# Performance work log

Measured on AMD Instinct MI355X. Metric: run time of the kernel, lower is better.

## Reference

```python
import jax, jax.numpy as jnp
import numpy as np
import math

N_HEADS = 16


def setup_inputs() -> dict:
    key = jax.random.key(0)
    ks = jax.random.split(key, 5)
    B, S, E = 2, 2048, 1024
    scale = 1.0 / math.sqrt(E)
    return {
        "x": jax.random.normal(ks[0], (B, S, E), dtype=jnp.float32),
        "w_in": jax.random.normal(ks[1], (3 * E, E), dtype=jnp.float32) * scale,
        "b_in": jax.random.normal(ks[2], (3 * E,), dtype=jnp.float32) * 0.01,
        "w_out": jax.random.normal(ks[3], (E, E), dtype=jnp.float32) * scale,
        "b_out": jax.random.normal(ks[4], (E,), dtype=jnp.float32) * 0.01,
    }


def reference(x, w_in, b_in, w_out, b_out):
    B, S, E = x.shape
    H = N_HEADS
    d = E // H
    # fused QKV projection: [B,S,3E]
    qkv = x @ w_in.T + b_in
    q, k, v = jnp.split(qkv, 3, axis=-1)
    # [B,S,E] -> [B,H,S,d]
    q = q.reshape(B, S, H, d).transpose(0, 2, 1, 3)
    k = k.reshape(B, S, H, d).transpose(0, 2, 1, 3)
    v = v.reshape(B, S, H, d).transpose(0, 2, 1, 3)
    # scores [B,H,S,S], scaled by 1/sqrt(d_head) (no causal mask: casual_mask=False)
    scores = jnp.einsum("bhqd,bhkd->bhqk", q, k) / jnp.sqrt(jnp.float32(d)).astype(x.dtype)
    w = jax.nn.softmax(scores, axis=-1)
    # attention output [B,H,S,d] -> [B,S,E]
    out = jnp.einsum("bhqk,bhkd->bhqd", w, v)
    out = out.transpose(0, 2, 1, 3).reshape(B, S, E)
    return out @ w_out.T + b_out
```

## Files before the change

kernel.cpp:

```cpp
#include <hip/hip_runtime.h>
#include <cstdint>


typedef __bf16 bf16x8 __attribute__((ext_vector_type(8)));
typedef short s16x4 __attribute__((ext_vector_type(4)));
typedef float f32x4 __attribute__((ext_vector_type(4)));

__device__ __forceinline__ unsigned short f32_to_bf16_rne(float f) {
    unsigned int u = __builtin_bit_cast(unsigned int, f);
    u += 0x7FFF + ((u >> 16) & 1);
    return (unsigned short)(u >> 16);
}

__device__ __forceinline__ unsigned int pack_bf16_trunc(float a, float b) {
    unsigned int ua = __builtin_bit_cast(unsigned int, a);
    unsigned int ub = __builtin_bit_cast(unsigned int, b);
    return __builtin_amdgcn_perm(ub, ua, 0x07060302u);
}

__device__ __forceinline__ void gload16(const void* g, void* l) {
    __builtin_amdgcn_global_load_lds(
        (const __attribute__((address_space(1))) unsigned int*)g,
        (__attribute__((address_space(3))) unsigned int*)l, 16, 0, 0);
}

__global__ void cvt_all(const float* __restrict__ x, const float* __restrict__ wi,
                        const float* __restrict__ wo, unsigned short* __restrict__ xb,
                        unsigned short* __restrict__ wib, unsigned short* __restrict__ wob) {
    int i = blockIdx.x * blockDim.x + threadIdx.x;
    const float* src; unsigned short* dst; int off;
    if (i < 1048576)            { src = x;  dst = xb;  off = i; }
    else if (i < 1048576 + 786432) { src = wi; dst = wib; off = i - 1048576; }
    else                        { src = wo; dst = wob; off = i - (1048576 + 786432); }
    float4 v = ((const float4*)src)[off];
    ushort4 o;
    o.x = f32_to_bf16_rne(v.x); o.y = f32_to_bf16_rne(v.y);
    o.z = f32_to_bf16_rne(v.z); o.w = f32_to_bf16_rne(v.w);
    ((ushort4*)dst)[off] = o;
}

__launch_bounds__(256)
__global__ void gemm_qkv(const unsigned short* __restrict__ X,
                         const unsigned short* __restrict__ W,
                         const float* __restrict__ bias,
                         unsigned short* __restrict__ Qp,
                         unsigned short* __restrict__ Kp,
                         unsigned short* __restrict__ Vt) {
    __shared__ __align__(16) unsigned short As[128 * 32];
    __shared__ __align__(16) unsigned short Bs[128 * 32];
    const int t = threadIdx.x;
    const int w = t >> 6, lane = t & 63, quad = lane >> 4, l16 = lane & 15;
    const int wm = (w >> 1) * 64, wn = (w & 1) * 64;
    const int m0 = blockIdx.y * 128, n0 = blockIdx.x * 128;

    f32x4 acc[4][4] = {};

    for (int kt = 0; kt < 1024; kt += 32) {
        __syncthreads();
#pragma unroll
        for (int i = 0; i < 2; ++i) {
            int c = t + 256 * i;
            int r = c >> 2, cc = (c & 3) * 8;
            gload16(&X[(m0 + r) * 1024 + kt + cc], &As[c * 8]);
            gload16(&W[(n0 + r) * 1024 + kt + cc], &Bs[c * 8]);
        }
        __syncthreads();
        bf16x8 af[4], bw[4];
#pragma unroll
        for (int mi = 0; mi < 4; ++mi)
            af[mi] = *(const bf16x8*)&As[(wm + mi * 16 + l16) * 32 + quad * 8];
#pragma unroll
        for (int ni = 0; ni < 4; ++ni)
            bw[ni] = *(const bf16x8*)&Bs[(wn + ni * 16 + l16) * 32 + quad * 8];
#pragma unroll
        for (int mi = 0; mi < 4; ++mi)
#pragma unroll
            for (int ni = 0; ni < 4; ++ni)
                acc[mi][ni] = __builtin_amdgcn_mfma_f32_16x16x32_bf16(af[mi], bw[ni], acc[mi][ni], 0, 0, 0);
    }

    const float QSCALE = 0.125f * 1.44269504089f;
#pragma unroll
    for (int mi = 0; mi < 4; ++mi) {
#pragma unroll
        for (int ni = 0; ni < 4; ++ni) {
            int col = n0 + wn + ni * 16 + l16;
            float bv = bias[col];
            int which = col >> 10;
            int hc = col & 1023;
            int h = hc >> 6, d = hc & 63;
            int row0 = m0 + wm + mi * 16 + quad * 4;
            int b = row0 >> 11, s0 = row0 & 2047;
            int bh = b * 16 + h;
            if (which == 2) {
                ushort4 pk;
                pk.x = f32_to_bf16_rne(acc[mi][ni][0] + bv);
                pk.y = f32_to_bf16_rne(acc[mi][ni][1] + bv);
                pk.z = f32_to_bf16_rne(acc[mi][ni][2] + bv);
                pk.w = f32_to_bf16_rne(acc[mi][ni][3] + bv);
                *(ushort4*)&Vt[(bh * 64 + d) * 2048 + s0] = pk;
            } else if (which == 0) {
#pragma unroll
                for (int r = 0; r < 4; ++r)
                    Qp[(bh * 2048 + s0 + r) * 64 + d] =
                        f32_to_bf16_rne((acc[mi][ni][r] + bv) * QSCALE);
            } else {
#pragma unroll
                for (int r = 0; r < 4; ++r)
                    Kp[(bh * 2048 + s0 + r) * 64 + d] = f32_to_bf16_rne(acc[mi][ni][r] + bv);
            }
        }
    }
}

#define LDP 72
__launch_bounds__(128, 2)
__global__ void attn(const unsigned short* __restrict__ Qp, const unsigned short* __restrict__ Kp,
                     const unsigned short* __restrict__ Vt, unsigned short* __restrict__ A2) {
    __shared__ __align__(16) unsigned short Ks[2][64 * LDP];
    __shared__ __align__(16) unsigned short Vs[2][64 * LDP];
    const int t = threadIdx.x, w = t >> 6, lane = t & 63, quad = lane >> 4, l16 = lane & 15;
    const int bh = blockIdx.x;
    const int qb = blockIdx.y;
    const unsigned short* Qh = Qp + bh * (2048 * 64);
    const unsigned short* Kh = Kp + bh * (2048 * 64);
    const unsigned short* Vh = Vt + bh * (64 * 2048);

    bf16x8 qf[2][2];
#pragma unroll
    for (int nq = 0; nq < 2; ++nq)
#pragma unroll
        for (int ks = 0; ks < 2; ++ks) {
            int row = qb * 64 + w * 32 + nq * 16 + l16;
            qf[nq][ks] = *(const bf16x8*)&Qh[row * 64 + ks * 32 + quad * 8];
        }

    f32x4 o_acc[4][2] = {};
    float l_lane[2] = {0.f, 0.f};

#pragma unroll
    for (int i = 0; i < 4; ++i) {
        int c = t + 128 * i;
        int r = c >> 3, cc = (c & 7) * 8;
        *(uint4*)&Ks[0][r * LDP + cc] = *(const uint4*)&Kh[r * 64 + cc];
        *(uint4*)&Vs[0][r * LDP + cc] = *(const uint4*)&Vh[r * 2048 + cc];
    }

    int cur = 0;
    for (int it = 0; it < 32; ++it) {
        __syncthreads();
        uint4 kn[4], vn[4];
        const bool pfetch = (it != 31);
        if (pfetch) {
            int ktn = (it + 1) * 64;
#pragma unroll
            for (int i = 0; i < 4; ++i) {
                int c = t + 128 * i;
                int r = c >> 3, cc = (c & 7) * 8;
                kn[i] = *(const uint4*)&Kh[(ktn + r) * 64 + cc];
                vn[i] = *(const uint4*)&Vh[r * 2048 + ktn + cc];
            }
        }
        const unsigned short* Kc = Ks[cur];
        const unsigned short* Vc = Vs[cur];

        f32x4 s_acc[4][2] = {};
#pragma unroll
        for (int ks = 0; ks < 2; ++ks)
#pragma unroll
            for (int mi = 0; mi < 4; ++mi) {
                bf16x8 kf = *(const bf16x8*)&Kc[(mi * 16 + l16) * LDP + ks * 32 + quad * 8];
#pragma unroll
                for (int nq = 0; nq < 2; ++nq)
                    s_acc[mi][nq] = __builtin_amdgcn_mfma_f32_16x16x32_bf16(kf, qf[nq][ks], s_acc[mi][nq], 0, 0, 0);
            }

        s16x4 bq[4][2];
#pragma unroll
        for (int nq = 0; nq < 2; ++nq) {
            float rsum = 0.f;
#pragma unroll
            for (int mi = 0; mi < 4; ++mi) {
                float p0 = exp2f(s_acc[mi][nq][0]);
                float p1 = exp2f(s_acc[mi][nq][1]);
                float p2 = exp2f(s_acc[mi][nq][2]);
                float p3 = exp2f(s_acc[mi][nq][3]);
                rsum += (p0 + p1) + (p2 + p3);
                uint2 pk;
                pk.x = pack_bf16_trunc(p0, p1);
                pk.y = pack_bf16_trunc(p2, p3);
                bq[mi][nq] = __builtin_bit_cast(s16x4, pk);
            }
            l_lane[nq] += rsum;
        }

#pragma unroll
        for (int dm = 0; dm < 4; ++dm)
#pragma unroll
            for (int kt4 = 0; kt4 < 4; ++kt4) {
                s16x4 av = __builtin_bit_cast(s16x4,
                    *(const uint2*)&Vc[(dm * 16 + l16) * LDP + kt4 * 16 + quad * 4]);
#pragma unroll
                for (int nq = 0; nq < 2; ++nq)
                    o_acc[dm][nq] = __builtin_amdgcn_mfma_f32_16x16x16bf16_1k(av, bq[kt4][nq], o_acc[dm][nq], 0, 0, 0);
            }

        if (pfetch) {
#pragma unroll
            for (int i = 0; i < 4; ++i) {
                int c = t + 128 * i;
                int r = c >> 3, cc = (c & 7) * 8;
                *(uint4*)&Ks[cur ^ 1][r * LDP + cc] = kn[i];
                *(uint4*)&Vs[cur ^ 1][r * LDP + cc] = vn[i];
            }
        }
        cur ^= 1;
    }

    const int b = bh >> 4, h = bh & 15;
#pragma unroll
    for (int nq = 0; nq < 2; ++nq) {
        float l = l_lane[nq];
        l += __shfl_xor(l, 16);
        l += __shfl_xor(l, 32);
        float rl = 1.0f / l;
        int s = qb * 64 + w * 32 + nq * 16 + l16;
        int tok = b * 2048 + s;
#pragma unroll
        for (int dm = 0; dm < 4; ++dm) {
            ushort4 o;
            o.x = f32_to_bf16_rne(o_acc[dm][nq][0] * rl);
            o.y = f32_to_bf16_rne(o_acc[dm][nq][1] * rl);
            o.z = f32_to_bf16_rne(o_acc[dm][nq][2] * rl);
            o.w = f32_to_bf16_rne(o_acc[dm][nq][3] * rl);
            *(ushort4*)&A2[tok * 1024 + h * 64 + dm * 16 + quad * 4] = o;
        }
    }
}

__launch_bounds__(256)
__global__ void gemm_out_k(const unsigned short* __restrict__ A, const unsigned short* __restrict__ W,
                           const float* __restrict__ bias, float* __restrict__ out) {
    __shared__ __align__(16) unsigned short As[128 * 32];
    __shared__ __align__(16) unsigned short Bs[64 * 32];
    const int t = threadIdx.x;
    const int w = t >> 6, lane = t & 63, quad = lane >> 4, l16 = lane & 15;
    const int wm = (w >> 1) * 64, wn = (w & 1) * 32;
    const int m0 = blockIdx.y * 128, n0 = blockIdx.x * 64;

    f32x4 acc[4][2] = {};

    for (int kt = 0; kt < 1024; kt += 32) {
        __syncthreads();
#pragma unroll
        for (int i = 0; i < 2; ++i) {
            int c = t + 256 * i;
            int r = c >> 2, cc = (c & 3) * 8;
            gload16(&A[(m0 + r) * 1024 + kt + cc], &As[c * 8]);
        }
        {
            int c = t;
            int r = c >> 2, cc = (c & 3) * 8;
            gload16(&W[(n0 + r) * 1024 + kt + cc], &Bs[c * 8]);
        }
        __syncthreads();
        bf16x8 af[4], bw[2];
#pragma unroll
        for (int mi = 0; mi < 4; ++mi)
            af[mi] = *(const bf16x8*)&As[(wm + mi * 16 + l16) * 32 + quad * 8];
#pragma unroll
        for (int ni = 0; ni < 2; ++ni)
            bw[ni] = *(const bf16x8*)&Bs[(wn + ni * 16 + l16) * 32 + quad * 8];
#pragma unroll
        for (int mi = 0; mi < 4; ++mi)
#pragma unroll
            for (int ni = 0; ni < 2; ++ni)
                acc[mi][ni] = __builtin_amdgcn_mfma_f32_16x16x32_bf16(af[mi], bw[ni], acc[mi][ni], 0, 0, 0);
    }

#pragma unroll
    for (int mi = 0; mi < 4; ++mi)
#pragma unroll
        for (int ni = 0; ni < 2; ++ni) {
            int col = n0 + wn + ni * 16 + l16;
            float bv = bias[col];
#pragma unroll
            for (int r = 0; r < 4; ++r) {
                int row = m0 + wm + mi * 16 + quad * 4 + r;
                out[row * 1024 + col] = acc[mi][ni][r] + bv;
            }
        }
}

extern "C" void kernel_launch(void* const* d_in, const int* in_sizes, int n_in,
                              void* d_out, int out_size, void* d_ws, size_t ws_size,
                              hipStream_t stream) {
    const float* x     = (const float*)d_in[0];
    const float* w_in  = (const float*)d_in[1];
    const float* b_in  = (const float*)d_in[2];
    const float* w_out = (const float*)d_in[3];
    const float* b_out = (const float*)d_in[4];
    float* out = (float*)d_out;

    char* ws = (char*)d_ws;
    unsigned short* xb  = (unsigned short*)(ws);
    unsigned short* wib = (unsigned short*)(ws + 8388608);
    unsigned short* wob = (unsigned short*)(ws + 14680064);
    unsigned short* Qp  = (unsigned short*)(ws + 16777216);
    unsigned short* Kp  = (unsigned short*)(ws + 25165824);
    unsigned short* Vt  = (unsigned short*)(ws + 33554432);
    unsigned short* A2  = (unsigned short*)(ws + 41943040);

    cvt_all<<<8192, 256, 0, stream>>>(x, w_in, w_out, xb, wib, wob);
    gemm_qkv<<<dim3(24, 32), 256, 0, stream>>>(xb, wib, b_in, Qp, Kp, Vt);
    attn<<<dim3(32, 32), 128, 0, stream>>>(Qp, Kp, Vt, A2);
    gemm_out_k<<<dim3(16, 32), 256, 0, stream>>>(A2, wob, b_out, out);
}
```

Before: 215.7 us.

## Deepen GEMM K-tiles, use direct-to-LDS swizzled loads in attention, fast exp2

```diff
diff --git a/kernel.cpp b/kernel.cpp
--- a/kernel.cpp
+++ b/kernel.cpp
@@ -46,8 +46,8 @@
                          unsigned short* __restrict__ Qp,
                          unsigned short* __restrict__ Kp,
                          unsigned short* __restrict__ Vt) {
-    __shared__ __align__(16) unsigned short As[128 * 32];
-    __shared__ __align__(16) unsigned short Bs[128 * 32];
+    __shared__ __align__(16) unsigned short As[128 * 64];
+    __shared__ __align__(16) unsigned short Bs[128 * 64];
     const int t = threadIdx.x;
     const int w = t >> 6, lane = t & 63, quad = lane >> 4, l16 = lane & 15;
     const int wm = (w >> 1) * 64, wn = (w & 1) * 64;
@@ -55,28 +55,31 @@
 
     f32x4 acc[4][4] = {};
 
-    for (int kt = 0; kt < 1024; kt += 32) {
-        __syncthreads();
-#pragma unroll
-        for (int i = 0; i < 2; ++i) {
+    for (int kt = 0; kt < 1024; kt += 64) {
+        __syncthreads();
+#pragma unroll
+        for (int i = 0; i < 4; ++i) {
             int c = t + 256 * i;
-            int r = c >> 2, cc = (c & 3) * 8;
+            int r = c >> 3, cc = (c & 7) * 8;
             gload16(&X[(m0 + r) * 1024 + kt + cc], &As[c * 8]);
             gload16(&W[(n0 + r) * 1024 + kt + cc], &Bs[c * 8]);
         }
         __syncthreads();
-        bf16x8 af[4], bw[4];
-#pragma unroll
-        for (int mi = 0; mi < 4; ++mi)
-            af[mi] = *(const bf16x8*)&As[(wm + mi * 16 + l16) * 32 + quad * 8];
-#pragma unroll
-        for (int ni = 0; ni < 4; ++ni)
-            bw[ni] = *(const bf16x8*)&Bs[(wn + ni * 16 + l16) * 32 + quad * 8];
-#pragma unroll
-        for (int mi = 0; mi < 4; ++mi)
+#pragma unroll
+        for (int ks = 0; ks < 2; ++ks) {
+            bf16x8 af[4], bw[4];
+#pragma unroll
+            for (int mi = 0; mi < 4; ++mi)
+                af[mi] = *(const bf16x8*)&As[(wm + mi * 16 + l16) * 64 + ks * 32 + quad * 8];
 #pragma unroll
             for (int ni = 0; ni < 4; ++ni)
-                acc[mi][ni] = __builtin_amdgcn_mfma_f32_16x16x32_bf16(af[mi], bw[ni], acc[mi][ni], 0, 0, 0);
+                bw[ni] = *(const bf16x8*)&Bs[(wn + ni * 16 + l16) * 64 + ks * 32 + quad * 8];
+#pragma unroll
+            for (int mi = 0; mi < 4; ++mi)
+#pragma unroll
+                for (int ni = 0; ni < 4; ++ni)
+                    acc[mi][ni] = __builtin_amdgcn_mfma_f32_16x16x32_bf16(af[mi], bw[ni], acc[mi][ni], 0, 0, 0);
+        }
     }
 
     const float QSCALE = 0.125f * 1.44269504089f;
@@ -113,12 +116,11 @@
     }
 }
 
-#define LDP 72
 __launch_bounds__(128, 2)
 __global__ void attn(const unsigned short* __restrict__ Qp, const unsigned short* __restrict__ Kp,
                      const unsigned short* __restrict__ Vt, unsigned short* __restrict__ A2) {
-    __shared__ __align__(16) unsigned short Ks[2][64 * LDP];
-    __shared__ __align__(16) unsigned short Vs[2][64 * LDP];
+    __shared__ __align__(16) unsigned short Ks[2][64 * 64];
+    __shared__ __align__(16) unsigned short Vs[2][64 * 64];
     const int t = threadIdx.x, w = t >> 6, lane = t & 63, quad = lane >> 4, l16 = lane & 15;
     const int bh = blockIdx.x;
     const int qb = blockIdx.y;
@@ -141,24 +143,22 @@
 #pragma unroll
     for (int i = 0; i < 4; ++i) {
         int c = t + 128 * i;
-        int r = c >> 3, cc = (c & 7) * 8;
-        *(uint4*)&Ks[0][r * LDP + cc] = *(const uint4*)&Kh[r * 64 + cc];
-        *(uint4*)&Vs[0][r * LDP + cc] = *(const uint4*)&Vh[r * 2048 + cc];
+        int r = c >> 3, sc = ((c & 7) ^ (r & 7)) << 3;
+        gload16(&Kh[r * 64 + sc], &Ks[0][c * 8]);
+        gload16(&Vh[r * 2048 + sc], &Vs[0][c * 8]);
     }
 
     int cur = 0;
     for (int it = 0; it < 32; ++it) {
         __syncthreads();
-        uint4 kn[4], vn[4];
-        const bool pfetch = (it != 31);
-        if (pfetch) {
+        if (it != 31) {
             int ktn = (it + 1) * 64;
 #pragma unroll
             for (int i = 0; i < 4; ++i) {
                 int c = t + 128 * i;
-                int r = c >> 3, cc = (c & 7) * 8;
-                kn[i] = *(const uint4*)&Kh[(ktn + r) * 64 + cc];
-                vn[i] = *(const uint4*)&Vh[r * 2048 + ktn + cc];
+                int r = c >> 3, sc = ((c & 7) ^ (r & 7)) << 3;
+                gload16(&Kh[(ktn + r) * 64 + sc], &Ks[cur ^ 1][c * 8]);
+                gload16(&Vh[r * 2048 + ktn + sc], &Vs[cur ^ 1][c * 8]);
             }
         }
         const unsigned short* Kc = Ks[cur];
@@ -169,7 +169,8 @@
         for (int ks = 0; ks < 2; ++ks)
 #pragma unroll
             for (int mi = 0; mi < 4; ++mi) {
-                bf16x8 kf = *(const bf16x8*)&Kc[(mi * 16 + l16) * LDP + ks * 32 + quad * 8];
+                bf16x8 kf = *(const bf16x8*)&Kc[(mi * 16 + l16) * 64 +
+                                                (((ks * 4 + quad) ^ (l16 & 7)) << 3)];
 #pragma unroll
                 for (int nq = 0; nq < 2; ++nq)
                     s_acc[mi][nq] = __builtin_amdgcn_mfma_f32_16x16x32_bf16(kf, qf[nq][ks], s_acc[mi][nq], 0, 0, 0);
@@ -181,10 +182,10 @@
             float rsum = 0.f;
 #pragma unroll
             for (int mi = 0; mi < 4; ++mi) {
-                float p0 = exp2f(s_acc[mi][nq][0]);
-                float p1 = exp2f(s_acc[mi][nq][1]);
-                float p2 = exp2f(s_acc[mi][nq][2]);
-                float p3 = exp2f(s_acc[mi][nq][3]);
+                float p0 = __builtin_amdgcn_exp2f(s_acc[mi][nq][0]);
+                float p1 = __builtin_amdgcn_exp2f(s_acc[mi][nq][1]);
+                float p2 = __builtin_amdgcn_exp2f(s_acc[mi][nq][2]);
+                float p3 = __builtin_amdgcn_exp2f(s_acc[mi][nq][3]);
                 rsum += (p0 + p1) + (p2 + p3);
                 uint2 pk;
                 pk.x = pack_bf16_trunc(p0, p1);
@@ -198,22 +199,13 @@
         for (int dm = 0; dm < 4; ++dm)
 #pragma unroll
             for (int kt4 = 0; kt4 < 4; ++kt4) {
+                int ch = (kt4 * 2 + (quad >> 1)) ^ (l16 & 7);
                 s16x4 av = __builtin_bit_cast(s16x4,
-                    *(const uint2*)&Vc[(dm * 16 + l16) * LDP + kt4 * 16 + quad * 4]);
+                    *(const uint2*)&Vc[(dm * 16 + l16) * 64 + (ch << 3) + (quad & 1) * 4]);
 #pragma unroll
                 for (int nq = 0; nq < 2; ++nq)
                     o_acc[dm][nq] = __builtin_amdgcn_mfma_f32_16x16x16bf16_1k(av, bq[kt4][nq], o_acc[dm][nq], 0, 0, 0);
             }
-
-        if (pfetch) {
-#pragma unroll
-            for (int i = 0; i < 4; ++i) {
-                int c = t + 128 * i;
-                int r = c >> 3, cc = (c & 7) * 8;
-                *(uint4*)&Ks[cur ^ 1][r * LDP + cc] = kn[i];
-                *(uint4*)&Vs[cur ^ 1][r * LDP + cc] = vn[i];
-            }
-        }
         cur ^= 1;
     }
 
@@ -241,8 +233,8 @@
 __launch_bounds__(256)
 __global__ void gemm_out_k(const unsigned short* __restrict__ A, const unsigned short* __restrict__ W,
                            const float* __restrict__ bias, float* __restrict__ out) {
-    __shared__ __align__(16) unsigned short As[128 * 32];
-    __shared__ __align__(16) unsigned short Bs[64 * 32];
+    __shared__ __align__(16) unsigned short As[128 * 64];
+    __shared__ __align__(16) unsigned short Bs[64 * 64];
     const int t = threadIdx.x;
     const int w = t >> 6, lane = t & 63, quad = lane >> 4, l16 = lane & 15;
     const int wm = (w >> 1) * 64, wn = (w & 1) * 32;
@@ -250,32 +242,36 @@
 
     f32x4 acc[4][2] = {};
 
-    for (int kt = 0; kt < 1024; kt += 32) {
-        __syncthreads();
+    for (int kt = 0; kt < 1024; kt += 64) {
+        __syncthreads();
+#pragma unroll
+        for (int i = 0; i < 4; ++i) {
+            int c = t + 256 * i;
+            int r = c >> 3, cc = (c & 7) * 8;
+            gload16(&A[(m0 + r) * 1024 + kt + cc], &As[c * 8]);
+        }
 #pragma unroll
         for (int i = 0; i < 2; ++i) {
             int c = t + 256 * i;
-            int r = c >> 2, cc = (c & 3) * 8;
-            gload16(&A[(m0 + r) * 1024 + kt + cc], &As[c * 8]);
-        }
-        {
-            int c = t;
-            int r = c >> 2, cc = (c & 3) * 8;
+            int r = c >> 3, cc = (c & 7) * 8;
             gload16(&W[(n0 + r) * 1024 + kt + cc], &Bs[c * 8]);
         }
         __syncthreads();
-        bf16x8 af[4], bw[2];
-#pragma unroll
-        for (int mi = 0; mi < 4; ++mi)
-            af[mi] = *(const bf16x8*)&As[(wm + mi * 16 + l16) * 32 + quad * 8];
-#pragma unroll
-        for (int ni = 0; ni < 2; ++ni)
-            bw[ni] = *(const bf16x8*)&Bs[(wn + ni * 16 + l16) * 32 + quad * 8];
-#pragma unroll
-        for (int mi = 0; mi < 4; ++mi)
+#pragma unroll
+        for (int ks = 0; ks < 2; ++ks) {
+            bf16x8 af[4], bw[2];
+#pragma unroll
+            for (int mi = 0; mi < 4; ++mi)
+                af[mi] = *(const bf16x8*)&As[(wm + mi * 16 + l16) * 64 + ks * 32 + quad * 8];
 #pragma unroll
             for (int ni = 0; ni < 2; ++ni)
-                acc[mi][ni] = __builtin_amdgcn_mfma_f32_16x16x32_bf16(af[mi], bw[ni], acc[mi][ni], 0, 0, 0);
+                bw[ni] = *(const bf16x8*)&Bs[(wn + ni * 16 + l16) * 64 + ks * 32 + quad * 8];
+#pragma unroll
+            for (int mi = 0; mi < 4; ++mi)
+#pragma unroll
+                for (int ni = 0; ni < 2; ++ni)
+                    acc[mi][ni] = __builtin_amdgcn_mfma_f32_16x16x32_bf16(af[mi], bw[ni], acc[mi][ni], 0, 0, 0);
+        }
     }
 
 #pragma unroll
```

Result: no change. 214.6 us (-0.5%).
